# Performance work log

Measured on AMD Instinct MI355X. Metric: run time of the kernel, lower is better.

Reference implementation:

```python
import jax, jax.numpy as jnp
import numpy as np

# Model constants (match init_kwargs)
P = 96        # patch_len (= stride)
D = 1024      # d_model
H = 8         # n_heads
DH = D // H   # head dim
EL = 8        # e_layers
DFF = 2048    # d_ff
EPS = 1e-5    # LayerNorm eps (torch default)


def _sinusoidal_pe(n, d):
    pos = np.arange(n)[:, None].astype(np.float32)
    div = np.exp(np.arange(0, d, 2).astype(np.float32) * (-np.log(10000.0) / d))
    pe = np.zeros((n, d), dtype=np.float32)
    pe[:, 0::2] = np.sin(pos * div)
    pe[:, 1::2] = np.cos(pos * div)
    return jnp.asarray(pe)


def _ln(x, g, b):
    m = jnp.mean(x, axis=-1, keepdims=True)
    v = jnp.mean(jnp.square(x - m), axis=-1, keepdims=True)
    return (x - m) * jax.lax.rsqrt(v + EPS) * g + b


def setup_inputs() -> dict:
    key = jax.random.key(0)
    ks = jax.random.split(key, 16)
    s = 0.02
    inp = {
        'x': jax.random.normal(ks[0], (4, 1, 1024 * P), dtype=jnp.float32),
        'W_emb': jax.random.normal(ks[1], (D, P), dtype=jnp.float32) * s,
        'Wq': jax.random.normal(ks[2], (EL, D, D), dtype=jnp.float32) * s,
        'bq': jnp.zeros((EL, D), jnp.float32),
        'Wk': jax.random.normal(ks[3], (EL, D, D), dtype=jnp.float32) * s,
        'bk': jnp.zeros((EL, D), jnp.float32),
        'Wv': jax.random.normal(ks[4], (EL, D, D), dtype=jnp.float32) * s,
        'bv': jnp.zeros((EL, D), jnp.float32),
        'Wo': jax.random.normal(ks[5], (EL, D, D), dtype=jnp.float32) * s,
        'bo': jnp.zeros((EL, D), jnp.float32),
        'Wc1': jax.random.normal(ks[6], (EL, DFF, D), dtype=jnp.float32) * s,
        'bc1': jnp.zeros((EL, DFF), jnp.float32),
        'Wc2': jax.random.normal(ks[7], (EL, D, DFF), dtype=jnp.float32) * s,
        'bc2': jnp.zeros((EL, D), jnp.float32),
        'g1': jnp.ones((EL, D), jnp.float32),
        'be1': jnp.zeros((EL, D), jnp.float32),
        'g2': jnp.ones((EL, D), jnp.float32),
        'be2': jnp.zeros((EL, D), jnp.float32),
        'gN': jnp.ones((D,), jnp.float32),
        'beN': jnp.zeros((D,), jnp.float32),
        'Wp': jax.random.normal(ks[8], (P, D), dtype=jnp.float32) * s,
        'bp': jnp.zeros((P,), jnp.float32),
    }
    return inp


def reference(x, W_emb, Wq, bq, Wk, bk, Wv, bv, Wo, bo, Wc1, bc1, Wc2, bc2,
              g1, be1, g2, be2, gN, beN, Wp, bp):
    B, V, T = x.shape
    N = T // P  # number of patches (stride == patch_len, padding == 0)
    BN = B * V
    # PatchEmbedding: unfold -> [B*V, N, P], linear embed (no bias) + sinusoidal PE
    tok = x.reshape(BN, N, P)
    h = jnp.einsum('bnp,dp->bnd', tok, W_emb) + _sinusoidal_pe(N, D)[None]
    # Causal mask (TriangularCausalMask): True above diagonal -> -inf
    causal = jnp.triu(jnp.ones((N, N), dtype=bool), k=1)
    scale = 1.0 / jnp.sqrt(jnp.float32(DH))
    for i in range(EL):
        q = (h @ Wq[i].T + bq[i]).reshape(BN, N, H, DH)
        k = (h @ Wk[i].T + bk[i]).reshape(BN, N, H, DH)
        v = (h @ Wv[i].T + bv[i]).reshape(BN, N, H, DH)
        scores = jnp.einsum('blhe,bshe->bhls', q, k)  # [BN,H,N,N]
        scores = jnp.where(causal, -jnp.inf, scores)
        A = jax.nn.softmax(scale * scores, axis=-1)
        att = jnp.einsum('bhls,bshd->blhd', A, v).reshape(BN, N, D)
        h = h + (att @ Wo[i].T + bo[i])            # residual (dropout=identity, eval)
        h = _ln(h, g1[i], be1[i])
        y = jax.nn.relu(h @ Wc1[i].T + bc1[i]) @ Wc2[i].T + bc2[i]  # kernel-1 convs == GEMMs
        h = _ln(h + y, g2[i], be2[i])
    h = _ln(h, gN, beN)  # Encoder final norm
    return h @ Wp.T + bp  # proj to patch_len: [B*V, N, P]
```

## Files before the change

### kernel.cpp

```cpp
#include <hip/hip_runtime.h>
#include <hip/hip_bf16.h>

typedef __attribute__((ext_vector_type(8))) short s8v;
typedef __attribute__((ext_vector_type(4))) float f4v;
typedef __attribute__((ext_vector_type(4))) short s4v;

__device__ __forceinline__ float b2f(short s) {
  unsigned int u = ((unsigned int)(unsigned short)s) << 16;
  return __builtin_bit_cast(float, u);
}
__device__ __forceinline__ short f2b(float f) {
  __hip_bfloat16 h = __float2bfloat16(f);
  return __builtin_bit_cast(short, h);
}

__device__ __forceinline__ void gload_lds16(const short* g, short* l) {
  __builtin_amdgcn_global_load_lds(
      (const __attribute__((address_space(1))) unsigned int*)g,
      (__attribute__((address_space(3))) unsigned int*)l, 16, 0, 0);
}

__global__ __launch_bounds__(256)
void cvt_f32_bf16(const float* __restrict__ in, short* __restrict__ out, int n) {
  int i = (blockIdx.x * 256 + threadIdx.x) * 4;
  if (i < n) {
    float4 v = *(const float4*)(in + i);
    s4v o = {f2b(v.x), f2b(v.y), f2b(v.z), f2b(v.w)};
    *(s4v*)(out + i) = o;
  }
}

__global__ __launch_bounds__(256)
void cvt_pack_w(const float* __restrict__ in, short* __restrict__ out, int base_off) {
  int i = (blockIdx.x * 256 + threadIdx.x) * 4;
  if (i < 8 * 1048576) {
    int layer = i >> 20, rem = i & 1048575;
    float4 v = *(const float4*)(in + i);
    s4v o = {f2b(v.x), f2b(v.y), f2b(v.z), f2b(v.w)};
    *(s4v*)(out + (size_t)layer * 3145728 + (size_t)base_off * 1024 + rem) = o;
  }
}

__global__ __launch_bounds__(256)
void pack_bias(const float* __restrict__ in, float* __restrict__ out, int off) {
  int i = blockIdx.x * 256 + threadIdx.x;
  if (i < 8192) {
    int layer = i >> 10, rem = i & 1023;
    out[layer * 3072 + off + rem] = in[i];
  }
}

__global__ __launch_bounds__(256, 2)
void gemm_bt(const short* __restrict__ A, const short* __restrict__ B,
             const float* __restrict__ bias, const float* res,
             float* outf, short* outb,
             int M, int N, int K, int ldc, int relu) {
  __shared__ short As[128 * 64];
  __shared__ short Bs[128 * 64];
  const int tid  = threadIdx.x;
  const int lane = tid & 63;
  const int w    = tid >> 6;
  const int wm   = w >> 1, wn = w & 1;
  const int llo  = lane & 15, g = lane >> 4;
  const int bm   = blockIdx.x, bn = blockIdx.y;

  const int srow = w * 32 + (lane >> 3);
  const int scol = (lane & 7) * 8;

  f4v acc[4][4];
#pragma unroll
  for (int i = 0; i < 4; ++i)
#pragma unroll
    for (int j = 0; j < 4; ++j) acc[i][j] = (f4v){0.f, 0.f, 0.f, 0.f};

  for (int k0 = 0; k0 < K; k0 += 64) {
    __syncthreads();
#pragma unroll
    for (int t = 0; t < 4; ++t) {
      int ar = bm * 128 + srow + t * 8;
      int br = bn * 128 + srow + t * 8; if (br >= N) br = N - 1;
      gload_lds16(A + (size_t)ar * K + k0 + scol, As + (w * 32 + t * 8) * 64);
      gload_lds16(B + (size_t)br * K + k0 + scol, Bs + (w * 32 + t * 8) * 64);
    }
    __syncthreads();
#pragma unroll
    for (int ks = 0; ks < 2; ++ks) {
      s8v a[4], b[4];
#pragma unroll
      for (int mi = 0; mi < 4; ++mi)
        a[mi] = *(const s8v*)&As[(wm * 64 + mi * 16 + llo) * 64 + ks * 32 + g * 8];
#pragma unroll
      for (int ni = 0; ni < 4; ++ni)
        b[ni] = *(const s8v*)&Bs[(wn * 64 + ni * 16 + llo) * 64 + ks * 32 + g * 8];
#pragma unroll
      for (int mi = 0; mi < 4; ++mi)
#pragma unroll
        for (int ni = 0; ni < 4; ++ni)
          acc[mi][ni] = __builtin_amdgcn_mfma_f32_16x16x32_bf16(a[mi], b[ni], acc[mi][ni], 0, 0, 0);
    }
  }

  const int r0 = bm * 128 + wm * 64;
  const int c0 = bn * 128 + wn * 64 + llo;
#pragma unroll
  for (int mi = 0; mi < 4; ++mi) {
#pragma unroll
    for (int ni = 0; ni < 4; ++ni) {
      int col = c0 + ni * 16;
      if (col < N) {
        float bv = bias ? bias[col] : 0.f;
#pragma unroll
        for (int r = 0; r < 4; ++r) {
          int row = r0 + mi * 16 + g * 4 + r;
          float v = acc[mi][ni][r] + bv;
          if (res)  v += res[(size_t)row * ldc + col];
          if (relu) v = fmaxf(v, 0.f);
          if (outf) outf[(size_t)row * ldc + col] = v;
          if (outb) outb[(size_t)row * ldc + col] = f2b(v);
        }
      }
    }
  }
}

__global__ __launch_bounds__(256, 2)
void gemm_bt64(const short* __restrict__ A, const short* __restrict__ B,
               const float* __restrict__ bias, const float* res,
               float* outf, short* outb,
               int M, int N, int K, int ldc, int relu) {
  __shared__ short As[64 * 64];
  __shared__ short Bs[128 * 64];
  const int tid  = threadIdx.x;
  const int lane = tid & 63;
  const int w    = tid >> 6;
  const int llo  = lane & 15, g = lane >> 4;
  const int bm   = blockIdx.x, bn = blockIdx.y;
  const int sr   = lane >> 3;
  const int scol = (lane & 7) * 8;

  f4v acc[4][2];
#pragma unroll
  for (int i = 0; i < 4; ++i)
#pragma unroll
    for (int j = 0; j < 2; ++j) acc[i][j] = (f4v){0.f, 0.f, 0.f, 0.f};

  for (int k0 = 0; k0 < K; k0 += 64) {
    __syncthreads();
#pragma unroll
    for (int t = 0; t < 2; ++t) {
      int ar = bm * 64 + w * 16 + t * 8 + sr;
      gload_lds16(A + (size_t)ar * K + k0 + scol, As + (w * 16 + t * 8) * 64);
    }
#pragma unroll
    for (int t = 0; t < 4; ++t) {
      int br = bn * 128 + w * 32 + t * 8 + sr; if (br >= N) br = N - 1;
      gload_lds16(B + (size_t)br * K + k0 + scol, Bs + (w * 32 + t * 8) * 64);
    }
    __syncthreads();
#pragma unroll
    for (int ks = 0; ks < 2; ++ks) {
      s8v a[4], b[2];
#pragma unroll
      for (int mi = 0; mi < 4; ++mi)
        a[mi] = *(const s8v*)&As[(mi * 16 + llo) * 64 + ks * 32 + g * 8];
#pragma unroll
      for (int ni = 0; ni < 2; ++ni)
        b[ni] = *(const s8v*)&Bs[(w * 32 + ni * 16 + llo) * 64 + ks * 32 + g * 8];
#pragma unroll
      for (int mi = 0; mi < 4; ++mi)
#pragma unroll
        for (int ni = 0; ni < 2; ++ni)
          acc[mi][ni] = __builtin_amdgcn_mfma_f32_16x16x32_bf16(a[mi], b[ni], acc[mi][ni], 0, 0, 0);
    }
  }

  const int r0 = bm * 64;
  const int c0 = bn * 128 + w * 32 + llo;
#pragma unroll
  for (int mi = 0; mi < 4; ++mi) {
#pragma unroll
    for (int ni = 0; ni < 2; ++ni) {
      int col = c0 + ni * 16;
      if (col < N) {
        float bv = bias ? bias[col] : 0.f;
#pragma unroll
        for (int r = 0; r < 4; ++r) {
          int row = r0 + mi * 16 + g * 4 + r;
          float v = acc[mi][ni][r] + bv;
          if (res)  v += res[(size_t)row * ldc + col];
          if (relu) v = fmaxf(v, 0.f);
          if (outf) outf[(size_t)row * ldc + col] = v;
          if (outb) outb[(size_t)row * ldc + col] = f2b(v);
        }
      }
    }
  }
}

#define ALD 136

__global__ __launch_bounds__(512, 1)
void attn_kernel(const short* __restrict__ qkv, short* __restrict__ att) {
  __shared__ short Ks[128 * ALD];
  __shared__ short Vt[128 * ALD];
  __shared__ short Ps[128 * ALD];
  const int tid = threadIdx.x;
  const int lane = tid & 63, w = tid >> 6;
  const int llo = lane & 15, g = lane >> 4;
  const int qt = blockIdx.x, hh = blockIdx.y, b = blockIdx.z;
  const float scale = 0.08838834764831845f;

  s8v qreg[4];
  {
    const short* qrow = qkv + (size_t)(b * 1024 + qt * 128 + w * 16 + llo) * 3072 + hh * 128;
#pragma unroll
    for (int ks = 0; ks < 4; ++ks) qreg[ks] = *(const s8v*)&qrow[ks * 32 + g * 8];
  }

  f4v o[8];
#pragma unroll
  for (int ni = 0; ni < 8; ++ni) o[ni] = (f4v){0.f, 0.f, 0.f, 0.f};
  float m_i[4], l_i[4];
#pragma unroll
  for (int r = 0; r < 4; ++r) { m_i[r] = -1e30f; l_i[r] = 0.f; }

  for (int kt = 0; kt <= qt; ++kt) {
    __syncthreads();
    const short* kbase = qkv + (size_t)(b * 1024 + kt * 128) * 3072 + 1024 + hh * 128;
    const short* vbase = qkv + (size_t)(b * 1024 + kt * 128) * 3072 + 2048 + hh * 128;
#pragma unroll
    for (int pass = 0; pass < 4; ++pass) {
      int chunk = pass * 512 + tid;
      int rr = chunk >> 4, c8 = (chunk & 15) * 8;
      *(s8v*)&Ks[rr * ALD + c8] = *(const s8v*)&kbase[(size_t)rr * 3072 + c8];
      int s = chunk & 127, d0 = (chunk >> 7) * 8;
      s8v vv = *(const s8v*)&vbase[(size_t)s * 3072 + d0];
#pragma unroll
      for (int j = 0; j < 8; ++j) Vt[(d0 + j) * ALD + s] = vv[j];
    }
    __syncthreads();

    f4v sc[8];
#pragma unroll
    for (int ni = 0; ni < 8; ++ni) sc[ni] = (f4v){0.f, 0.f, 0.f, 0.f};
#pragma unroll
    for (int ks = 0; ks < 4; ++ks) {
#pragma unroll
      for (int ni = 0; ni < 8; ++ni) {
        s8v bk = *(const s8v*)&Ks[(ni * 16 + llo) * ALD + ks * 32 + g * 8];
        sc[ni] = __builtin_amdgcn_mfma_f32_16x16x32_bf16(qreg[ks], bk, sc[ni], 0, 0, 0);
      }
    }

    const bool diag = (kt == qt);
#pragma unroll
    for (int r = 0; r < 4; ++r) {
      int rowl = w * 16 + g * 4 + r;
      float mx = -1e30f;
#pragma unroll
      for (int ni = 0; ni < 8; ++ni) {
        float v = sc[ni][r] * scale;
        if (diag && (ni * 16 + llo) > rowl) v = -1e30f;
        sc[ni][r] = v;
        mx = fmaxf(mx, v);
      }
      mx = fmaxf(mx, __shfl_xor(mx, 1, 64));
      mx = fmaxf(mx, __shfl_xor(mx, 2, 64));
      mx = fmaxf(mx, __shfl_xor(mx, 4, 64));
      mx = fmaxf(mx, __shfl_xor(mx, 8, 64));
      float mnew  = fmaxf(m_i[r], mx);
      float alpha = __expf(m_i[r] - mnew);
      m_i[r] = mnew;
      float rs = 0.f;
#pragma unroll
      for (int ni = 0; ni < 8; ++ni) {
        float p = __expf(sc[ni][r] - mnew);
        rs += p;
        Ps[rowl * ALD + ni * 16 + llo] = f2b(p);
      }
      rs += __shfl_xor(rs, 1, 64);
      rs += __shfl_xor(rs, 2, 64);
      rs += __shfl_xor(rs, 4, 64);
      rs += __shfl_xor(rs, 8, 64);
      l_i[r] = l_i[r] * alpha + rs;
#pragma unroll
      for (int ni = 0; ni < 8; ++ni) o[ni][r] *= alpha;
    }

#pragma unroll
    for (int ks = 0; ks < 4; ++ks) {
      s8v ap = *(const s8v*)&Ps[(w * 16 + llo) * ALD + ks * 32 + g * 8];
#pragma unroll
      for (int ni = 0; ni < 8; ++ni) {
        s8v bv = *(const s8v*)&Vt[(ni * 16 + llo) * ALD + ks * 32 + g * 8];
        o[ni] = __builtin_amdgcn_mfma_f32_16x16x32_bf16(ap, bv, o[ni], 0, 0, 0);
      }
    }
  }

#pragma unroll
  for (int r = 0; r < 4; ++r) {
    float inv = 1.f / l_i[r];
    size_t obase = (size_t)(b * 1024 + qt * 128 + w * 16 + g * 4 + r) * 1024 + hh * 128;
#pragma unroll
    for (int ni = 0; ni < 8; ++ni)
      att[obase + ni * 16 + llo] = f2b(o[ni][r] * inv);
  }
}

__global__ __launch_bounds__(256)
void ln_kernel(const float* in, const float* __restrict__ gw,
               const float* __restrict__ bw, float* outf,
               short* __restrict__ outb) {
  const int row = blockIdx.x, tid = threadIdx.x;
  const int lane = tid & 63, w = tid >> 6;
  float4 v = *(const float4*)(in + (size_t)row * 1024 + tid * 4);
  float s = v.x + v.y + v.z + v.w;
  float q = v.x * v.x + v.y * v.y + v.z * v.z + v.w * v.w;
  for (int off = 1; off < 64; off <<= 1) {
    s += __shfl_xor(s, off, 64);
    q += __shfl_xor(q, off, 64);
  }
  __shared__ float red[8];
  if (lane == 0) { red[w] = s; red[4 + w] = q; }
  __syncthreads();
  s = red[0] + red[1] + red[2] + red[3];
  q = red[4] + red[5] + red[6] + red[7];
  const float mean = s * (1.0f / 1024.0f);
  const float var  = q * (1.0f / 1024.0f) - mean * mean;
  const float rstd = rsqrtf(var + 1e-5f);
  const int d = tid * 4;
  float4 gv = *(const float4*)(gw + d);
  float4 bv = *(const float4*)(bw + d);
  float o0 = (v.x - mean) * rstd * gv.x + bv.x;
  float o1 = (v.y - mean) * rstd * gv.y + bv.y;
  float o2 = (v.z - mean) * rstd * gv.z + bv.z;
  float o3 = (v.w - mean) * rstd * gv.w + bv.w;
  if (outf) {
    float4 ov = {o0, o1, o2, o3};
    *(float4*)(outf + (size_t)row * 1024 + d) = ov;
  }
  s4v ob = {f2b(o0), f2b(o1), f2b(o2), f2b(o3)};
  *(s4v*)(outb + (size_t)row * 1024 + d) = ob;
}

__global__ __launch_bounds__(256)
void embed_kernel(const float* __restrict__ x, const short* __restrict__ Wemb,
                  float* __restrict__ hf, short* __restrict__ hb) {
  __shared__ float Xs[4 * 96];
  const int tid = threadIdx.x;
  const int m0  = blockIdx.x * 4;
  for (int i = tid; i < 4 * 96; i += 256) Xs[i] = x[(size_t)m0 * 96 + i];
  __syncthreads();

  const int d0 = tid * 4;
  float acc[4][4];
#pragma unroll
  for (int j = 0; j < 4; ++j)
#pragma unroll
    for (int t = 0; t < 4; ++t) acc[j][t] = 0.f;

  for (int pc = 0; pc < 12; ++pc) {
    float wf[4][8];
#pragma unroll
    for (int j = 0; j < 4; ++j) {
      s8v wv = *(const s8v*)&Wemb[(size_t)(d0 + j) * 96 + pc * 8];
#pragma unroll
      for (int u = 0; u < 8; ++u) wf[j][u] = b2f(wv[u]);
    }
#pragma unroll
    for (int t = 0; t < 4; ++t) {
      float4 xa = *(const float4*)&Xs[t * 96 + pc * 8];
      float4 xb = *(const float4*)&Xs[t * 96 + pc * 8 + 4];
      float xv[8] = {xa.x, xa.y, xa.z, xa.w, xb.x, xb.y, xb.z, xb.w};
#pragma unroll
      for (int u = 0; u < 8; ++u)
#pragma unroll
        for (int j = 0; j < 4; ++j) acc[j][t] += xv[u] * wf[j][u];
    }
  }

  const float kfreq = -0.008994473019508041f;
  float freq0 = __expf((float)d0 * kfreq);
  float freq2 = __expf((float)(d0 + 2) * kfreq);
#pragma unroll
  for (int t = 0; t < 4; ++t) {
    int n = (m0 + t) & 1023;
    float s0, c0, s2, c2;
    sincosf((float)n * freq0, &s0, &c0);
    sincosf((float)n * freq2, &s2, &c2);
    float o0 = acc[0][t] + s0;
    float o1 = acc[1][t] + c0;
    float o2 = acc[2][t] + s2;
    float o3 = acc[3][t] + c2;
    float4 ov = {o0, o1, o2, o3};
    *(float4*)(hf + (size_t)(m0 + t) * 1024 + d0) = ov;
    s4v ob = {f2b(o0), f2b(o1), f2b(o2), f2b(o3)};
    *(s4v*)(hb + (size_t)(m0 + t) * 1024 + d0) = ob;
  }
}

extern "C" void kernel_launch(void* const* d_in, const int* in_sizes, int n_in,
                              void* d_out, int out_size, void* d_ws, size_t ws_size,
                              hipStream_t stream) {
  (void)in_sizes; (void)n_in; (void)out_size; (void)ws_size;
  const float* x    = (const float*)d_in[0];
  const float* Wemb = (const float*)d_in[1];
  const float* Wq   = (const float*)d_in[2];
  const float* bq   = (const float*)d_in[3];
  const float* Wk   = (const float*)d_in[4];
  const float* bk   = (const float*)d_in[5];
  const float* Wv   = (const float*)d_in[6];
  const float* bv   = (const float*)d_in[7];
  const float* Wo   = (const float*)d_in[8];
  const float* bo   = (const float*)d_in[9];
  const float* Wc1  = (const float*)d_in[10];
  const float* bc1  = (const float*)d_in[11];
  const float* Wc2  = (const float*)d_in[12];
  const float* bc2  = (const float*)d_in[13];
  const float* g1   = (const float*)d_in[14];
  const float* be1  = (const float*)d_in[15];
  const float* g2   = (const float*)d_in[16];
  const float* be2  = (const float*)d_in[17];
  const float* gN   = (const float*)d_in[18];
  const float* beN  = (const float*)d_in[19];
  const float* Wp   = (const float*)d_in[20];
  const float* bp   = (const float*)d_in[21];

  char* wsc = (char*)d_ws;
  const size_t MB = 1024 * 1024;
  short* wqkv_b = (short*)(wsc + 0 * MB);
  short* wo_b   = (short*)(wsc + 48 * MB);
  short* wc1_b  = (short*)(wsc + 64 * MB);
  short* wc2_b  = (short*)(wsc + 96 * MB);
  short* wemb_b = (short*)(wsc + 128 * MB);
  short* wp_b   = (short*)(wsc + 128 * MB + 196608);
  float* bqkv   = (float*)(wsc + 128 * MB + 393216);
  float* h_f32  = (float*)(wsc + 129 * MB);
  short* h_bf   = (short*)(wsc + 145 * MB);
  short* qkv    = (short*)(wsc + 153 * MB);
  short* att    = (short*)(wsc + 177 * MB);
  short* y1     = qkv;

  cvt_pack_w<<<8192, 256, 0, stream>>>(Wq, wqkv_b, 0);
  cvt_pack_w<<<8192, 256, 0, stream>>>(Wk, wqkv_b, 1024);
  cvt_pack_w<<<8192, 256, 0, stream>>>(Wv, wqkv_b, 2048);
  pack_bias<<<32, 256, 0, stream>>>(bq, bqkv, 0);
  pack_bias<<<32, 256, 0, stream>>>(bk, bqkv, 1024);
  pack_bias<<<32, 256, 0, stream>>>(bv, bqkv, 2048);
  cvt_f32_bf16<<<8192, 256, 0, stream>>>(Wo, wo_b, 8 * 1024 * 1024);
  cvt_f32_bf16<<<16384, 256, 0, stream>>>(Wc1, wc1_b, 16 * 1024 * 1024);
  cvt_f32_bf16<<<16384, 256, 0, stream>>>(Wc2, wc2_b, 16 * 1024 * 1024);
  cvt_f32_bf16<<<96, 256, 0, stream>>>(Wemb, wemb_b, 98304);
  cvt_f32_bf16<<<96, 256, 0, stream>>>(Wp, wp_b, 98304);

  embed_kernel<<<1024, 256, 0, stream>>>(x, wemb_b, h_f32, h_bf);

  for (int i = 0; i < 8; ++i) {
    const short* wqkv = wqkv_b + (size_t)i * 3072 * 1024;
    const short* wo = wo_b + (size_t)i * 1024 * 1024;
    const short* w1 = wc1_b + (size_t)i * 2048 * 1024;
    const short* w2 = wc2_b + (size_t)i * 1024 * 2048;

    gemm_bt<<<dim3(32, 24), 256, 0, stream>>>(h_bf, wqkv, bqkv + i * 3072, nullptr,
                                              nullptr, qkv, 4096, 3072, 1024, 3072, 0);
    attn_kernel<<<dim3(8, 8, 4), 512, 0, stream>>>(qkv, att);
    gemm_bt64<<<dim3(64, 8), 256, 0, stream>>>(att, wo, bo + i * 1024, h_f32,
                                               h_f32, nullptr, 4096, 1024, 1024, 1024, 0);
    ln_kernel<<<4096, 256, 0, stream>>>(h_f32, g1 + i * 1024, be1 + i * 1024, h_f32, h_bf);
    gemm_bt<<<dim3(32, 16), 256, 0, stream>>>(h_bf, w1, bc1 + i * 2048, nullptr,
                                              nullptr, y1, 4096, 2048, 1024, 2048, 1);
    gemm_bt64<<<dim3(64, 8), 256, 0, stream>>>(y1, w2, bc2 + i * 1024, h_f32,
                                               h_f32, nullptr, 4096, 1024, 2048, 1024, 0);
    ln_kernel<<<4096, 256, 0, stream>>>(h_f32, g2 + i * 1024, be2 + i * 1024, h_f32, h_bf);
  }

  ln_kernel<<<4096, 256, 0, stream>>>(h_f32, gN, beN, nullptr, h_bf);
  gemm_bt64<<<dim3(64, 1), 256, 0, stream>>>(h_bf, wp_b, bp, nullptr,
                                             (float*)d_out, nullptr, 4096, 96, 1024, 96, 0);
}
```

Before: 2.186 ms.

## Merge weight-conversion launches and run patch embedding through the MFMA GEMM

Merges the separate weight-conversion and bias-packing launches into fewer combined kernels, which cuts the number of kernel launches in the prologue. The scalar embed kernel is replaced by zero-padding x and W_emb from 96 to 128 columns, precomputing the sinusoidal PE table in a separate kernel, and running the existing bf16 MFMA gemm_bt with PE as the residual input. The gemm residual index now wraps the row modulo 1024, which is correct here because the later residual calls use only 4096x1024 h buffers whose rows repeat every 1024? Actually no: the later calls pass h_f32 as a residual with 4096 rows, so wrapping breaks them if gemm_bt is used with res elsewhere; the layer loop only calls gemm_bt64 with a residual, so it is safe. The padding wastes some compute and the bias-packing kernel combines three inputs into one launch.

Measured after the change: 2.151 ms. About the same (-1.6%).

```diff
diff --git a/kernel.cpp b/kernel.cpp
--- a/kernel.cpp
+++ b/kernel.cpp
@@ -31,23 +31,69 @@
 }
 
 __global__ __launch_bounds__(256)
-void cvt_pack_w(const float* __restrict__ in, short* __restrict__ out, int base_off) {
-  int i = (blockIdx.x * 256 + threadIdx.x) * 4;
-  if (i < 8 * 1048576) {
-    int layer = i >> 20, rem = i & 1048575;
-    float4 v = *(const float4*)(in + i);
+void cvt_pack_qkv(const float* __restrict__ Wq, const float* __restrict__ Wk,
+                  const float* __restrict__ Wv, short* __restrict__ out) {
+  int c = blockIdx.x * 256 + threadIdx.x;
+  int which = c >> 21;
+  int i = (c & ((1 << 21) - 1)) * 4;
+  const float* in = which == 0 ? Wq : (which == 1 ? Wk : Wv);
+  int layer = i >> 20, rem = i & 1048575;
+  float4 v = *(const float4*)(in + i);
+  s4v o = {f2b(v.x), f2b(v.y), f2b(v.z), f2b(v.w)};
+  *(s4v*)(out + (size_t)layer * 3145728 + (size_t)which * 1048576 + rem) = o;
+}
+
+__global__ __launch_bounds__(256)
+void cvt_w3(const float* __restrict__ Wo, const float* __restrict__ Wc1,
+            const float* __restrict__ Wc2, short* __restrict__ wo_b,
+            short* __restrict__ wc1_b, short* __restrict__ wc2_b) {
+  int c = blockIdx.x * 256 + threadIdx.x;
+  const float* in; short* out; int i;
+  if (c < (1 << 21))            { in = Wo;  out = wo_b;  i = c * 4; }
+  else if (c < 6 * (1 << 20))   { in = Wc1; out = wc1_b; i = (c - (1 << 21)) * 4; }
+  else                          { in = Wc2; out = wc2_b; i = (c - 6 * (1 << 20)) * 4; }
+  float4 v = *(const float4*)(in + i);
+  s4v o = {f2b(v.x), f2b(v.y), f2b(v.z), f2b(v.w)};
+  *(s4v*)(out + i) = o;
+}
+
+__global__ __launch_bounds__(256)
+void pack_bias3(const float* __restrict__ bq, const float* __restrict__ bk,
+                const float* __restrict__ bv, float* __restrict__ out) {
+  int i = blockIdx.x * 256 + threadIdx.x;
+  int which = i >> 13, rem = i & 8191;
+  const float* in = which == 0 ? bq : (which == 1 ? bk : bv);
+  int layer = rem >> 10, r = rem & 1023;
+  out[layer * 3072 + which * 1024 + r] = in[rem];
+}
+
+__global__ __launch_bounds__(256)
+void pad96(const float* __restrict__ in, short* __restrict__ out, int rows) {
+  int idx = blockIdx.x * 256 + threadIdx.x;
+  if (idx >= rows * 32) return;
+  int r = idx >> 5, c = (idx & 31) * 4;
+  if (c < 96) {
+    float4 v = *(const float4*)(in + (size_t)r * 96 + c);
     s4v o = {f2b(v.x), f2b(v.y), f2b(v.z), f2b(v.w)};
-    *(s4v*)(out + (size_t)layer * 3145728 + (size_t)base_off * 1024 + rem) = o;
-  }
-}
-
-__global__ __launch_bounds__(256)
-void pack_bias(const float* __restrict__ in, float* __restrict__ out, int off) {
-  int i = blockIdx.x * 256 + threadIdx.x;
-  if (i < 8192) {
-    int layer = i >> 10, rem = i & 1023;
-    out[layer * 3072 + off + rem] = in[i];
-  }
+    *(s4v*)(out + (size_t)r * 128 + c) = o;
+  } else {
+    s4v z = {0, 0, 0, 0};
+    *(s4v*)(out + (size_t)r * 128 + c) = z;
+  }
+}
+
+__global__ __launch_bounds__(256)
+void pe_kernel(float* __restrict__ pe) {
+  int n = blockIdx.x;
+  int d0 = threadIdx.x * 4;
+  const float kfreq = -0.008994473019508041f;
+  float f0 = __expf((float)d0 * kfreq);
+  float f2 = __expf((float)(d0 + 2) * kfreq);
+  float s0, c0, s2, c2;
+  sincosf((float)n * f0, &s0, &c0);
+  sincosf((float)n * f2, &s2, &c2);
+  float4 v = {s0, c0, s2, c2};
+  *(float4*)(pe + (size_t)n * 1024 + d0) = v;
 }
 
 __global__ __launch_bounds__(256, 2)
@@ -113,7 +159,7 @@
         for (int r = 0; r < 4; ++r) {
           int row = r0 + mi * 16 + g * 4 + r;
           float v = acc[mi][ni][r] + bv;
-          if (res)  v += res[(size_t)row * ldc + col];
+          if (res)  v += res[(size_t)(row & 1023) * ldc + col];
           if (relu) v = fmaxf(v, 0.f);
           if (outf) outf[(size_t)row * ldc + col] = v;
           if (outb) outb[(size_t)row * ldc + col] = f2b(v);
@@ -342,62 +388,6 @@
   }
   s4v ob = {f2b(o0), f2b(o1), f2b(o2), f2b(o3)};
   *(s4v*)(outb + (size_t)row * 1024 + d) = ob;
-}
-
-__global__ __launch_bounds__(256)
-void embed_kernel(const float* __restrict__ x, const short* __restrict__ Wemb,
-                  float* __restrict__ hf, short* __restrict__ hb) {
-  __shared__ float Xs[4 * 96];
-  const int tid = threadIdx.x;
-  const int m0  = blockIdx.x * 4;
-  for (int i = tid; i < 4 * 96; i += 256) Xs[i] = x[(size_t)m0 * 96 + i];
-  __syncthreads();
-
-  const int d0 = tid * 4;
-  float acc[4][4];
-#pragma unroll
-  for (int j = 0; j < 4; ++j)
-#pragma unroll
-    for (int t = 0; t < 4; ++t) acc[j][t] = 0.f;
-
-  for (int pc = 0; pc < 12; ++pc) {
-    float wf[4][8];
-#pragma unroll
-    for (int j = 0; j < 4; ++j) {
-      s8v wv = *(const s8v*)&Wemb[(size_t)(d0 + j) * 96 + pc * 8];
-#pragma unroll
-      for (int u = 0; u < 8; ++u) wf[j][u] = b2f(wv[u]);
-    }
-#pragma unroll
-    for (int t = 0; t < 4; ++t) {
-      float4 xa = *(const float4*)&Xs[t * 96 + pc * 8];
-      float4 xb = *(const float4*)&Xs[t * 96 + pc * 8 + 4];
-      float xv[8] = {xa.x, xa.y, xa.z, xa.w, xb.x, xb.y, xb.z, xb.w};
-#pragma unroll
-      for (int u = 0; u < 8; ++u)
-#pragma unroll
-        for (int j = 0; j < 4; ++j) acc[j][t] += xv[u] * wf[j][u];
-    }
-  }
-
-  const float kfreq = -0.008994473019508041f;
-  float freq0 = __expf((float)d0 * kfreq);
-  float freq2 = __expf((float)(d0 + 2) * kfreq);
-#pragma unroll
-  for (int t = 0; t < 4; ++t) {
-    int n = (m0 + t) & 1023;
-    float s0, c0, s2, c2;
-    sincosf((float)n * freq0, &s0, &c0);
-    sincosf((float)n * freq2, &s2, &c2);
-    float o0 = acc[0][t] + s0;
-    float o1 = acc[1][t] + c0;
-    float o2 = acc[2][t] + s2;
-    float o3 = acc[3][t] + c2;
-    float4 ov = {o0, o1, o2, o3};
-    *(float4*)(hf + (size_t)(m0 + t) * 1024 + d0) = ov;
-    s4v ob = {f2b(o0), f2b(o1), f2b(o2), f2b(o3)};
-    *(s4v*)(hb + (size_t)(m0 + t) * 1024 + d0) = ob;
-  }
 }
 
 extern "C" void kernel_launch(void* const* d_in, const int* in_sizes, int n_in,
@@ -433,28 +423,27 @@
   short* wo_b   = (short*)(wsc + 48 * MB);
   short* wc1_b  = (short*)(wsc + 64 * MB);
   short* wc2_b  = (short*)(wsc + 96 * MB);
-  short* wemb_b = (short*)(wsc + 128 * MB);
-  short* wp_b   = (short*)(wsc + 128 * MB + 196608);
-  float* bqkv   = (float*)(wsc + 128 * MB + 393216);
+  short* wembp  = (short*)(wsc + 128 * MB);
+  short* wp_b   = (short*)(wsc + 128 * MB + 262144);
+  float* bqkv   = (float*)(wsc + 128 * MB + 458752);
   float* h_f32  = (float*)(wsc + 129 * MB);
   short* h_bf   = (short*)(wsc + 145 * MB);
   short* qkv    = (short*)(wsc + 153 * MB);
   short* att    = (short*)(wsc + 177 * MB);
   short* y1     = qkv;
-
-  cvt_pack_w<<<8192, 256, 0, stream>>>(Wq, wqkv_b, 0);
-  cvt_pack_w<<<8192, 256, 0, stream>>>(Wk, wqkv_b, 1024);
-  cvt_pack_w<<<8192, 256, 0, stream>>>(Wv, wqkv_b, 2048);
-  pack_bias<<<32, 256, 0, stream>>>(bq, bqkv, 0);
-  pack_bias<<<32, 256, 0, stream>>>(bk, bqkv, 1024);
-  pack_bias<<<32, 256, 0, stream>>>(bv, bqkv, 2048);
-  cvt_f32_bf16<<<8192, 256, 0, stream>>>(Wo, wo_b, 8 * 1024 * 1024);
-  cvt_f32_bf16<<<16384, 256, 0, stream>>>(Wc1, wc1_b, 16 * 1024 * 1024);
-  cvt_f32_bf16<<<16384, 256, 0, stream>>>(Wc2, wc2_b, 16 * 1024 * 1024);
-  cvt_f32_bf16<<<96, 256, 0, stream>>>(Wemb, wemb_b, 98304);
+  short* xpad   = qkv;
+  float* pe     = (float*)att;
+
+  cvt_pack_qkv<<<24576, 256, 0, stream>>>(Wq, Wk, Wv, wqkv_b);
+  cvt_w3<<<40960, 256, 0, stream>>>(Wo, Wc1, Wc2, wo_b, wc1_b, wc2_b);
+  pack_bias3<<<96, 256, 0, stream>>>(bq, bk, bv, bqkv);
   cvt_f32_bf16<<<96, 256, 0, stream>>>(Wp, wp_b, 98304);
-
-  embed_kernel<<<1024, 256, 0, stream>>>(x, wemb_b, h_f32, h_bf);
+  pad96<<<512, 256, 0, stream>>>(x, xpad, 4096);
+  pad96<<<128, 256, 0, stream>>>(Wemb, wembp, 1024);
+  pe_kernel<<<1024, 256, 0, stream>>>(pe);
+
+  gemm_bt<<<dim3(32, 8), 256, 0, stream>>>(xpad, wembp, nullptr, pe,
+                                           h_f32, h_bf, 4096, 1024, 128, 1024, 0);
 
   for (int i = 0; i < 8; ++i) {
     const short* wqkv = wqkv_b + (size_t)i * 3072 * 1024;
```
